# Kernel tuning notes

Hardware: AMD Instinct MI355X
Metric: run time of the kernel (lower is better)

The kernel has to match this reference:

```python
import jax, jax.numpy as jnp
import numpy as np

N_STATE = 64
N_LAYERS = 4
D_MODEL = 512
D_OUT = 256
BATCH = 16
SEQLEN = 2048


def setup_inputs() -> dict:
    key = jax.random.key(0)
    ks = jax.random.split(key, 16)
    H, N, nl = D_MODEL, N_STATE, N_LAYERS
    inp = {}
    inp["x"] = jax.random.normal(ks[0], (BATCH, SEQLEN, D_MODEL), dtype=jnp.float32)
    # encoder / decoder dense
    inp["enc_w"] = jax.random.normal(ks[1], (D_MODEL, D_MODEL), jnp.float32) / np.sqrt(D_MODEL)
    inp["enc_b"] = jnp.zeros((D_MODEL,), jnp.float32)
    inp["dec_w"] = jax.random.normal(ks[2], (D_MODEL, D_OUT), jnp.float32) / np.sqrt(D_MODEL)
    inp["dec_b"] = jnp.zeros((D_OUT,), jnp.float32)
    # per-layer LayerNorm
    inp["ln_scale"] = jnp.ones((nl, D_MODEL), jnp.float32)
    inp["ln_bias"] = jnp.zeros((nl, D_MODEL), jnp.float32)
    # per-layer S4 DPLR params (stored as real/imag float pairs)
    inp["lambda_re"] = -0.5 * jnp.ones((nl, H, N), jnp.float32)
    inp["lambda_im"] = jnp.broadcast_to(np.pi * jnp.arange(N, dtype=jnp.float32), (nl, H, N))
    inp["p_re"] = jax.random.normal(ks[3], (nl, H, N), jnp.float32) * 0.5
    inp["p_im"] = jax.random.normal(ks[4], (nl, H, N), jnp.float32) * 0.5
    inp["b_re"] = jax.random.normal(ks[5], (nl, H, N), jnp.float32) * 0.5
    inp["b_im"] = jax.random.normal(ks[6], (nl, H, N), jnp.float32) * 0.5
    inp["c_re"] = jax.random.normal(ks[7], (nl, H, N), jnp.float32) * 0.5
    inp["c_im"] = jax.random.normal(ks[8], (nl, H, N), jnp.float32) * 0.5
    inp["log_step"] = jax.random.uniform(ks[9], (nl, H), jnp.float32, minval=np.log(1e-3), maxval=np.log(1e-1))
    inp["d_param"] = jnp.ones((nl, H), jnp.float32)
    # per-layer output Dense
    inp["out_w"] = jax.random.normal(ks[10], (nl, D_MODEL, D_MODEL), jnp.float32) / np.sqrt(D_MODEL)
    inp["out_b"] = jnp.zeros((nl, D_MODEL), jnp.float32)
    return inp


def _layer_norm(x, scale, bias, eps=1e-6):
    mu = jnp.mean(x, axis=-1, keepdims=True)
    var = jnp.mean(jnp.square(x - mu), axis=-1, keepdims=True)
    return (x - mu) * jax.lax.rsqrt(var + eps) * scale + bias


def _kernel_dplr(Lam, P, B, C, step, L):
    # Lam,P,B,C: [H,N] complex64; step: [H] float32 -> K: [H,L] float32
    theta = (2.0 * np.pi / L) * jnp.arange(L, dtype=jnp.float32)
    Omega = jnp.exp(-1j * theta)                        # [L] roots of unity
    g = (2.0 / step)[:, None] * ((1.0 - Omega) / (1.0 + Omega))[None, :]  # [H,L]
    c = 2.0 / (1.0 + Omega)                             # [L]
    r = 1.0 / (g[:, :, None] - Lam[:, None, :])         # [H,L,N] resolvent (Cauchy)
    Cc, Pc = jnp.conj(C), jnp.conj(P)
    k00 = jnp.einsum("hn,hln->hl", Cc * B, r)
    k01 = jnp.einsum("hn,hln->hl", Cc * P, r)
    k10 = jnp.einsum("hn,hln->hl", Pc * B, r)
    k11 = jnp.einsum("hn,hln->hl", Pc * P, r)
    at_roots = c[None, :] * (k00 - k01 * (1.0 / (1.0 + k11)) * k10)  # [H,L]
    return jnp.fft.ifft(at_roots, n=L, axis=-1).real


def _s4_apply(u, Lam, P, B, C, step, D):
    # u: [Bt,L,H]; causal FFT convolution with kernel K[h,:] per channel
    L = u.shape[1]
    K = _kernel_dplr(Lam, P, B, C, step, L)             # [H,L]
    ud = jnp.fft.rfft(u, n=2 * L, axis=1)               # [Bt,L+1,H]
    Kd = jnp.fft.rfft(K, n=2 * L, axis=-1)              # [H,L+1]
    y = jnp.fft.irfft(ud * Kd.T[None], n=2 * L, axis=1)[:, :L]
    return y + D[None, None, :] * u


def reference(x, enc_w, enc_b, ln_scale, ln_bias, lambda_re, lambda_im,
              p_re, p_im, b_re, b_im, c_re, c_im, log_step, d_param,
              out_w, out_b, dec_w, dec_b):
    h = x @ enc_w + enc_b
    n_layers = ln_scale.shape[0]
    for i in range(n_layers):
        skip = h
        z = _layer_norm(h, ln_scale[i], ln_bias[i])
        Lam = lambda_re[i] + 1j * lambda_im[i]
        P = p_re[i] + 1j * p_im[i]
        B = b_re[i] + 1j * b_im[i]
        C = c_re[i] + 1j * c_im[i]
        z = _s4_apply(z, Lam, P, B, C, jnp.exp(log_step[i]), d_param[i])
        z = jax.nn.gelu(z)
        z = z @ out_w[i] + out_b[i]
        h = skip + z  # dropout=0.0 -> identity
    logits = h @ dec_w + dec_b
    return jax.nn.log_softmax(logits, axis=-1)
```

## Files before the change

kernel.cpp:

```cpp
#include <hip/hip_runtime.h>
#include <hip/hip_bf16.h>

#define NLAY 4
#define DH   512
#define NST  64
#define NB   16
#define SL   2048
#define NDO  256
#define BL   (NB*SL)
#define KDIM 512
#define TWOPI 6.283185307179586476925287

typedef unsigned short u16;
typedef __attribute__((ext_vector_type(8))) short  short8v;
typedef __attribute__((ext_vector_type(8))) unsigned short ushort8v;
typedef __attribute__((ext_vector_type(4))) float  f32x4;

#define RCPF(x) __builtin_amdgcn_rcpf(x)

__device__ __forceinline__ float bf2f(u16 v){
  union { unsigned u; float f; } x; x.u = ((unsigned)v) << 16; return x.f;
}
__device__ __forceinline__ u16 f2bf(float f){
  union { float f; unsigned u; } x; x.f = f;
  unsigned u = x.u;
  unsigned r = u + 0x7fffu + ((u >> 16) & 1u);
  return (u16)(r >> 16);
}
__device__ __forceinline__ void cmulw(float& xr, float& xi, float wr, float wi){
  float tr = xr*wr - xi*wi;
  xi = fmaf(xr, wi, xi*wr);
  xr = tr;
}
__device__ __forceinline__ float gelu_fast(float v){
  const float c0 = 0.7978845608028654f;
  float u = c0 * fmaf(0.044715f, v*v*v, v);
  return v * RCPF(1.0f + __expf(-2.0f * u));
}

template<int SGN>
__device__ __forceinline__ void dft4w(float& r0, float& i0, float& r1, float& i1,
                                      float& r2, float& i2, float& r3, float& i3){
  const float t0r = r0 + r2, t0i = i0 + i2;
  const float t1r = r0 - r2, t1i = i0 - i2;
  const float t2r = r1 + r3, t2i = i1 + i3;
  const float t3r = r1 - r3, t3i = i1 - i3;
  r0 = t0r + t2r; i0 = t0i + t2i;
  r2 = t0r - t2r; i2 = t0i - t2i;
  if (SGN < 0){ r1 = t1r + t3i; i1 = t1i - t3r; r3 = t1r - t3i; i3 = t1i + t3r; }
  else        { r1 = t1r - t3i; i1 = t1i + t3r; r3 = t1r + t3i; i3 = t1i - t3r; }
}

template<int SGN>
__device__ __forceinline__ void dft16(float* re, float* im){
#pragma unroll
  for (int b = 0; b < 4; b++)
    dft4w<SGN>(re[b], im[b], re[4+b], im[4+b], re[8+b], im[8+b], re[12+b], im[12+b]);
  const float C1 = 0.92387953251128675613f, S1_ = 0.38268343236508977172f;
  const float C2 = 0.70710678118654752440f;
  const float sg = (SGN < 0) ? -1.f : 1.f;
  cmulw(re[5],  im[5],   C1,  sg*S1_);
  cmulw(re[9],  im[9],   C2,  sg*C2);
  cmulw(re[13], im[13],  S1_, sg*C1);
  cmulw(re[6],  im[6],   C2,  sg*C2);
  cmulw(re[10], im[10],  0.f, sg*1.f);
  cmulw(re[14], im[14], -C2,  sg*C2);
  cmulw(re[7],  im[7],   S1_, sg*C1);
  cmulw(re[11], im[11], -C2,  sg*C2);
  cmulw(re[15], im[15], -C1,  sg*(-S1_));
#pragma unroll
  for (int c = 0; c < 4; c++)
    dft4w<SGN>(re[4*c], im[4*c], re[4*c+1], im[4*c+1], re[4*c+2], im[4*c+2], re[4*c+3], im[4*c+3]);
  float tr_, ti_;
#define SWP(A,B) tr_=re[A]; re[A]=re[B]; re[B]=tr_; ti_=im[A]; im[A]=im[B]; im[B]=ti_;
  SWP(1,4) SWP(2,8) SWP(3,12) SWP(6,9) SWP(7,13) SWP(11,14)
#undef SWP
}

__device__ __forceinline__ int cxpad(int i){ return i + (i >> 4) + ((i >> 8) << 1); }
#define CXSZ 4384

__device__ __forceinline__ void fwd4096(float* re, float* im, float2* cx, int t){
  dft16<-1>(re, im);
  const float a0 = -(float)(TWOPI/4096.0) * (float)t;
#pragma unroll
  for (int k = 0; k < 16; k++){
    if (k){ float sn = __sinf(a0*(float)k), cs = __cosf(a0*(float)k); cmulw(re[k], im[k], cs, sn); }
    cx[cxpad(t + 256*k)] = make_float2(re[k], im[k]);
  }
  __syncthreads();
  const int k1 = t >> 4, m2 = t & 15;
  const int b2 = k1*256 + m2;
#pragma unroll
  for (int j = 0; j < 16; j++){ float2 v = cx[cxpad(b2 + 16*j)]; re[j] = v.x; im[j] = v.y; }
  dft16<-1>(re, im);
  const float b0 = -(float)(TWOPI/256.0) * (float)m2;
#pragma unroll
  for (int k = 0; k < 16; k++){
    if (k){ float sn = __sinf(b0*(float)k), cs = __cosf(b0*(float)k); cmulw(re[k], im[k], cs, sn); }
    cx[cxpad(b2 + 16*k)] = make_float2(re[k], im[k]);
  }
  __syncthreads();
#pragma unroll
  for (int j = 0; j < 16; j++){ float2 v = cx[cxpad(16*t + j)]; re[j] = v.x; im[j] = v.y; }
  dft16<-1>(re, im);
}

__device__ __forceinline__ void inv4096(float* re, float* im, float2* cx, int t){
  dft16<1>(re, im);
#pragma unroll
  for (int j = 0; j < 16; j++) cx[cxpad(16*t + j)] = make_float2(re[j], im[j]);
  __syncthreads();
  const int k1 = t >> 4, m2 = t & 15;
  const int b2 = k1*256 + m2;
  const float b0 = (float)(TWOPI/256.0) * (float)m2;
#pragma unroll
  for (int k = 0; k < 16; k++){
    float2 v = cx[cxpad(b2 + 16*k)];
    re[k] = v.x; im[k] = v.y;
    if (k){ float sn = __sinf(b0*(float)k), cs = __cosf(b0*(float)k); cmulw(re[k], im[k], cs, sn); }
  }
  dft16<1>(re, im);
#pragma unroll
  for (int j = 0; j < 16; j++) cx[cxpad(b2 + 16*j)] = make_float2(re[j], im[j]);
  __syncthreads();
  const float a0 = (float)(TWOPI/4096.0) * (float)t;
#pragma unroll
  for (int k = 0; k < 16; k++){
    float2 v = cx[cxpad(t + 256*k)];
    re[k] = v.x; im[k] = v.y;
    if (k){ float sn = __sinf(a0*(float)k), cs = __cosf(a0*(float)k); cmulw(re[k], im[k], cs, sn); }
  }
  dft16<1>(re, im);
}

__global__ __launch_bounds__(256) void prep_k(
  const float* __restrict__ lam_re, const float* __restrict__ lam_im,
  const float* __restrict__ p_re,  const float* __restrict__ p_im,
  const float* __restrict__ b_re,  const float* __restrict__ b_im,
  const float* __restrict__ c_re,  const float* __restrict__ c_im,
  float4* __restrict__ cwA, float4* __restrict__ cwB, float* __restrict__ cwS)
{
  const int i = blockIdx.x * 256 + threadIdx.x;
  const float lr = lam_re[i], li = lam_im[i];
  const float pr = p_re[i],  pi = p_im[i];
  const float br = b_re[i],  bi = b_im[i];
  const float cr = c_re[i],  ci = c_im[i];
  cwA[i] = make_float4(lr, li, cr*br + ci*bi, cr*bi - ci*br);
  cwB[i] = make_float4(cr*pr + ci*pi, cr*pi - ci*pr, pr*br + pi*bi, pr*bi - pi*br);
  cwS[i] = pr*pr + pi*pi;
}

__global__ __launch_bounds__(256) void cauchy_k(
    const float4* __restrict__ cwA, const float4* __restrict__ cwB,
    const float* __restrict__ cwS, const float* __restrict__ lstep,
    float2* __restrict__ Kd)
{
  const int t = threadIdx.x;
  const int h = blockIdx.y, lay = blockIdx.z;
  const int l = blockIdx.x * 256 + t;
  const int wb = (lay*DH + h) * NST;
  const float stp = expf(lstep[lay*DH + h]);
  const float tw0 = 2.0f / stp;

  const float th = (float)(TWOPI/2048.0) * (float)l;
  const float sn = sinf(th), cs = cosf(th);
  const float omr = cs, omi = -sn;
  const float a1r = 1.f - omr, a1i = -omi;
  const float a2r = 1.f + omr, a2i =  omi;
  const float inv2 = RCPF(fmaf(a2r, a2r, a2i*a2i));
  const float gr = tw0 * fmaf(a1r, a2r,  a1i*a2i) * inv2;
  const float gi = tw0 * fmaf(a1i, a2r, -a1r*a2i) * inv2;
  const float clr = 2.f * a2r * inv2, cli = -2.f * a2i * inv2;

  float k00r=0.f,k00i=0.f,k01r=0.f,k01i=0.f,k10r=0.f,k10i=0.f,k11r=0.f,k11i=0.f;
#pragma unroll 4
  for (int n = 0; n < NST; n++){
    const float4 A  = cwA[wb + n];
    const float4 Bv = cwB[wb + n];
    const float w11 = cwS[wb + n];
    const float dr = gr - A.x, di = gi - A.y;
    const float s = RCPF(fmaf(dr, dr, di*di));
    const float ivr = dr * s, ivi = -di * s;
    k00r = fmaf(A.z, ivr, fmaf(-A.w, ivi, k00r)); k00i = fmaf(A.z, ivi, fmaf(A.w, ivr, k00i));
    k01r = fmaf(Bv.x,ivr, fmaf(-Bv.y,ivi, k01r)); k01i = fmaf(Bv.x,ivi, fmaf(Bv.y,ivr, k01i));
    k10r = fmaf(Bv.z,ivr, fmaf(-Bv.w,ivi, k10r)); k10i = fmaf(Bv.z,ivi, fmaf(Bv.w,ivr, k10i));
    k11r = fmaf(w11, ivr, k11r);                  k11i = fmaf(w11, ivi, k11i);
  }
  const float d1r = 1.f + k11r, d1i = k11i;
  const float idn = RCPF(fmaf(d1r, d1r, d1i*d1i));
  const float wr = k01r*k10r - k01i*k10i, wi = k01r*k10i + k01i*k10r;
  const float vr = fmaf(wr, d1r,  wi*d1i) * idn;
  const float vi = fmaf(wi, d1r, -wr*d1i) * idn;
  const float sr = k00r - vr, si = k00i - vi;
  Kd[(size_t)(lay*DH + h) * 4096 + l] =
      make_float2(clr*sr - cli*si, fmaf(clr, si, cli*sr));
}

__global__ __launch_bounds__(256) void kdfft_k(float2* __restrict__ Kd){
  __shared__ float  ar[SL], ai[SL];
  __shared__ float2 cx[CXSZ];
  const int t = threadIdx.x;
  const size_t base = (size_t)blockIdx.x * 4096;
#pragma unroll
  for (int q = 0; q < 8; q++){
    const int l = t + 256*q;
    float2 v = Kd[base + l];
    const int brv = __brev((unsigned)l) >> 21;
    ar[brv] = v.x; ai[brv] = v.y;
  }
  __syncthreads();

  for (int s = 0; s < 11; s++){
    const int half = 1 << s;
    const float fac = (float)(TWOPI) / (float)(2 << s);
#pragma unroll
    for (int q = 0; q < 4; q++){
      const int v = t + 256*q;
      const int pos = v & (half - 1);
      const int i0 = ((v >> s) << (s+1)) + pos;
      const int i1 = i0 + half;
      const float ang = fac * (float)pos;
      const float wc = __cosf(ang), ws = __sinf(ang);
      const float xr = ar[i1], xi = ai[i1];
      const float tr = wc*xr - ws*xi, ti = fmaf(wc, xi, ws*xr);
      const float ur_ = ar[i0], ui_ = ai[i0];
      ar[i0] = ur_ + tr; ai[i0] = ui_ + ti;
      ar[i1] = ur_ - tr; ai[i1] = ui_ - ti;
    }
    __syncthreads();
  }

  float re[16], im[16];
#pragma unroll
  for (int j = 0; j < 16; j++){
    re[j] = (j < 8) ? ar[t + 256*j] * (1.0f/2048.f) : 0.f;
    im[j] = 0.f;
  }
  fwd4096(re, im, cx, t);
  float2* kp = Kd + base + 16*t;
#pragma unroll
  for (int k = 0; k < 16; k += 2)
    *(float4*)(kp + k) = make_float4(re[k], im[k], re[k+1], im[k+1]);
}

__global__ __launch_bounds__(256) void wconv_k(const float* __restrict__ src,
    u16* __restrict__ dst, int K, int N){
  __shared__ u16 tile[64][72];
  const size_t mb = (size_t)blockIdx.z * K * N;
  const int k0 = blockIdx.x * 64, n0 = blockIdx.y * 64;
  const int r = threadIdx.x >> 2, c4 = (threadIdx.x & 3) * 16;
  const float* s = src + mb + (size_t)(k0 + r) * N + n0 + c4;
  float4 f0 = *(const float4*)s, f1 = *(const float4*)(s+4);
  float4 f2 = *(const float4*)(s+8), f3 = *(const float4*)(s+12);
  tile[c4+0][r]=f2bf(f0.x); tile[c4+1][r]=f2bf(f0.y); tile[c4+2][r]=f2bf(f0.z); tile[c4+3][r]=f2bf(f0.w);
  tile[c4+4][r]=f2bf(f1.x); tile[c4+5][r]=f2bf(f1.y); tile[c4+6][r]=f2bf(f1.z); tile[c4+7][r]=f2bf(f1.w);
  tile[c4+8][r]=f2bf(f2.x); tile[c4+9][r]=f2bf(f2.y); tile[c4+10][r]=f2bf(f2.z); tile[c4+11][r]=f2bf(f2.w);
  tile[c4+12][r]=f2bf(f3.x); tile[c4+13][r]=f2bf(f3.y); tile[c4+14][r]=f2bf(f3.z); tile[c4+15][r]=f2bf(f3.w);
  __syncthreads();
  u16* d = dst + mb + (size_t)(n0 + r) * K + k0 + c4;
  *(ushort8v*)d       = *(const ushort8v*)&tile[r][c4];
  *(ushort8v*)(d + 8) = *(const ushort8v*)&tile[r][c4 + 8];
}

__global__ __launch_bounds__(256) void ln_k(const float* __restrict__ hsrc,
    const float* __restrict__ gam, const float* __restrict__ bet,
    u16* __restrict__ zdst){
  const int row = blockIdx.x * 4 + (threadIdx.x >> 6);
  const int lane = threadIdx.x & 63;
  const float* p = hsrc + (size_t)row * DH + lane * 8;
  float4 a = *(const float4*)p, b = *(const float4*)(p + 4);
  float s  = (a.x + a.y) + (a.z + a.w) + (b.x + b.y) + (b.z + b.w);
  float sq = a.x*a.x + a.y*a.y + a.z*a.z + a.w*a.w
           + b.x*b.x + b.y*b.y + b.z*b.z + b.w*b.w;
#pragma unroll
  for (int o = 32; o; o >>= 1){ s += __shfl_xor(s, o); sq += __shfl_xor(sq, o); }
  const float mu = s * (1.0f/DH);
  const float rs = rsqrtf(sq * (1.0f/DH) - mu*mu + 1e-6f);
  const float4 g0 = *(const float4*)(gam + lane*8), g1 = *(const float4*)(gam + lane*8 + 4);
  const float4 t0 = *(const float4*)(bet + lane*8), t1 = *(const float4*)(bet + lane*8 + 4);
  ushort8v o;
  o[0] = f2bf(fmaf((a.x - mu)*rs, g0.x, t0.x));
  o[1] = f2bf(fmaf((a.y - mu)*rs, g0.y, t0.y));
  o[2] = f2bf(fmaf((a.z - mu)*rs, g0.z, t0.z));
  o[3] = f2bf(fmaf((a.w - mu)*rs, g0.w, t0.w));
  o[4] = f2bf(fmaf((b.x - mu)*rs, g1.x, t1.x));
  o[5] = f2bf(fmaf((b.y - mu)*rs, g1.y, t1.y));
  o[6] = f2bf(fmaf((b.z - mu)*rs, g1.z, t1.z));
  o[7] = f2bf(fmaf((b.w - mu)*rs, g1.w, t1.w));
  *(ushort8v*)(zdst + (size_t)row * DH + lane*8) = o;
}

__global__ __launch_bounds__(256) void transp_k(const u16* __restrict__ z,
                                                u16* __restrict__ zT){
  __shared__ u16 tile[64][72];
  const int bz = blockIdx.z;
  const int l0 = blockIdx.x * 64, h0 = blockIdx.y * 64;
  const int r = threadIdx.x >> 2, c4 = (threadIdx.x & 3) * 16;
  const u16* src = z + ((size_t)bz * SL + l0 + r) * DH + h0 + c4;
  ushort8v v0 = *(const ushort8v*)src;
  ushort8v v1 = *(const ushort8v*)(src + 8);
#pragma unroll
  for (int j = 0; j < 8; j++){ tile[c4 + j][r] = v0[j]; tile[c4 + 8 + j][r] = v1[j]; }
  __syncthreads();
  u16* dst = zT + ((size_t)bz * DH + h0 + r) * SL + l0 + c4;
  *(ushort8v*)dst       = *(const ushort8v*)&tile[r][c4];
  *(ushort8v*)(dst + 8) = *(const ushort8v*)&tile[r][c4 + 8];
}

__global__ __launch_bounds__(256) void s4conv_k(
    const u16* __restrict__ zT, const float2* __restrict__ Kd,
    const float* __restrict__ dpar, u16* __restrict__ yT)
{
  __shared__ float2 cx[CXSZ];
  const int t = threadIdx.x;
  const int wg = blockIdx.x;
  const int h = wg & 511, bp = wg >> 9;
  const u16* r1 = zT + ((size_t)(2*bp) * DH + h) * SL;
  const u16* r2 = r1 + (size_t)DH * SL;
  float ur1[8], ur2[8];
  float re[16], im[16];
#pragma unroll
  for (int j = 0; j < 8; j++){
    ur1[j] = bf2f(r1[t + 256*j]);
    ur2[j] = bf2f(r2[t + 256*j]);
    re[j] = ur1[j]; im[j] = ur2[j];
  }
#pragma unroll
  for (int j = 8; j < 16; j++){ re[j] = 0.f; im[j] = 0.f; }

  fwd4096(re, im, cx, t);

  const float2* kp = Kd + (size_t)h * 4096 + 16*t;
#pragma unroll
  for (int k = 0; k < 16; k += 2){
    float4 w2 = *(const float4*)(kp + k);
    cmulw(re[k],   im[k],   w2.x, w2.y);
    cmulw(re[k+1], im[k+1], w2.z, w2.w);
  }

  inv4096(re, im, cx, t);

  const float Dv = dpar[h];
  u16* y1 = yT + ((size_t)(2*bp) * DH + h) * SL;
  u16* y2 = y1 + (size_t)DH * SL;
#pragma unroll
  for (int j = 0; j < 8; j++){
    float v1 = fmaf(re[j], (1.0f/4096.f), Dv * ur1[j]);
    float v2 = fmaf(im[j], (1.0f/4096.f), Dv * ur2[j]);
    y1[t + 256*j] = f2bf(gelu_fast(v1));
    y2[t + 256*j] = f2bf(gelu_fast(v2));
  }
}

template<int AMODE, bool RESID>
__global__ __launch_bounds__(256) void gemm_k(
    const void* __restrict__ Aptr, const u16* __restrict__ Wt,
    const float* __restrict__ bias,
    const float* __restrict__ resid, float* __restrict__ Cout,
    int Mb, int N)
{
  __shared__ u16 As[128][40];
  __shared__ u16 Bs[128][40];
  const int t = threadIdx.x;
  const int n0 = blockIdx.x * 128, m0 = blockIdx.y * 128, bb = blockIdx.z;
  const int lane = t & 63, wv = t >> 6;
  const int wm = (wv >> 1) * 64, wn = (wv & 1) * 64;
  f32x4 acc[4][4];
#pragma unroll
  for (int mi = 0; mi < 4; mi++)
#pragma unroll
    for (int ni = 0; ni < 4; ni++) acc[mi][ni] = {0.f, 0.f, 0.f, 0.f};

  const u16*  Ab = (const u16*)Aptr;
  const float* Af = (const float*)Aptr;
  const size_t Abase = (AMODE == 1) ? (size_t)bb * KDIM * Mb : 0;

  for (int k0 = 0; k0 < KDIM; k0 += 32){
    __syncthreads();
    if (AMODE == 1){
      const int kk = t >> 3, ch = t & 7;
      const u16* srca = Ab + Abase + (size_t)(k0 + kk) * Mb + m0 + ch*16;
      ushort8v v0 = *(const ushort8v*)srca;
      ushort8v v1 = *(const ushort8v*)(srca + 8);
      const int col = (kk & 7) | (((kk >> 3) ^ (ch & 3)) << 3);
#pragma unroll
      for (int i = 0; i < 8; i++){
        As[ch*16 + i][col]     = (u16)v0[i];
        As[ch*16 + 8 + i][col] = (u16)v1[i];
      }
    } else if (AMODE == 0){
      const int r = t >> 1, kh = (t & 1) << 4;
      const u16* srca = Ab + (size_t)(m0 + r) * KDIM + k0 + kh;
      ushort8v v0 = *(const ushort8v*)srca;
      ushort8v v1 = *(const ushort8v*)(srca + 8);
      const int s3 = (r >> 4) & 3;
      const int c0 = (((kh >> 3) ^ s3) << 3);
      const int c1 = ((((kh >> 3) + 1) ^ s3) << 3);
      *(ushort8v*)&As[r][c0] = v0;
      *(ushort8v*)&As[r][c1] = v1;
    } else {
      const int r = t >> 1, kh = (t & 1) << 4;
      const float* sf = Af + (size_t)(m0 + r) * KDIM + k0 + kh;
      float4 f0 = *(const float4*)sf,     f1 = *(const float4*)(sf + 4);
      float4 f2 = *(const float4*)(sf+8), f3 = *(const float4*)(sf + 12);
      ushort8v v0, v1;
      v0[0]=f2bf(f0.x); v0[1]=f2bf(f0.y); v0[2]=f2bf(f0.z); v0[3]=f2bf(f0.w);
      v0[4]=f2bf(f1.x); v0[5]=f2bf(f1.y); v0[6]=f2bf(f1.z); v0[7]=f2bf(f1.w);
      v1[0]=f2bf(f2.x); v1[1]=f2bf(f2.y); v1[2]=f2bf(f2.z); v1[3]=f2bf(f2.w);
      v1[4]=f2bf(f3.x); v1[5]=f2bf(f3.y); v1[6]=f2bf(f3.z); v1[7]=f2bf(f3.w);
      const int s3 = (r >> 4) & 3;
      const int c0 = (((kh >> 3) ^ s3) << 3);
      const int c1 = ((((kh >> 3) + 1) ^ s3) << 3);
      *(ushort8v*)&As[r][c0] = v0;
      *(ushort8v*)&As[r][c1] = v1;
    }
    {
      const int r = t >> 1, kh = (t & 1) << 4;
      const u16* srcb = Wt + (size_t)(n0 + r) * KDIM + k0 + kh;
      ushort8v v0 = *(const ushort8v*)srcb;
      ushort8v v1 = *(const ushort8v*)(srcb + 8);
      const int s3 = (r >> 4) & 3;
      const int c0 = (((kh >> 3) ^ s3) << 3);
      const int c1 = ((((kh >> 3) + 1) ^ s3) << 3);
      *(ushort8v*)&Bs[r][c0] = v0;
      *(ushort8v*)&Bs[r][c1] = v1;
    }
    __syncthreads();

    const int ko = (lane >> 4) * 8;
    const int fr = lane & 15;
    short8v af[4], bf[4];
#pragma unroll
    for (int mi = 0; mi < 4; mi++){
      const int col = (((ko >> 3) ^ (((wm >> 4) + mi) & 3)) << 3);
      af[mi] = *(const short8v*)&As[wm + mi*16 + fr][col];
    }
#pragma unroll
    for (int ni = 0; ni < 4; ni++){
      const int col = (((ko >> 3) ^ (((wn >> 4) + ni) & 3)) << 3);
      bf[ni] = *(const short8v*)&Bs[wn + ni*16 + fr][col];
    }
#pragma unroll
    for (int mi = 0; mi < 4; mi++)
#pragma unroll
      for (int ni = 0; ni < 4; ni++)
        acc[mi][ni] = __builtin_amdgcn_mfma_f32_16x16x32_bf16(af[mi], bf[ni], acc[mi][ni], 0, 0, 0);
  }

  const int fr = lane & 15;
  const int rq = (lane >> 4) * 4;
#pragma unroll
  for (int mi = 0; mi < 4; mi++){
#pragma unroll
    for (int ni = 0; ni < 4; ni++){
      const int gn = n0 + wn + ni*16 + fr;
      const float bs = bias[gn];
#pragma unroll
      for (int q = 0; q < 4; q++){
        const int gm = m0 + wm + mi*16 + rq + q;
        const size_t idx = ((size_t)bb * Mb + gm) * N + gn;
        float v = acc[mi][ni][q] + bs;
        if (RESID) v += resid[idx];
        Cout[idx] = v;
      }
    }
  }
}

__global__ __launch_bounds__(256) void lsm_k(float* __restrict__ o){
  const int row = blockIdx.x * 4 + (threadIdx.x >> 6);
  const int lane = threadIdx.x & 63;
  float* p = o + (size_t)row * NDO + lane * 4;
  float4 v = *(const float4*)p;
  float mx = fmaxf(fmaxf(v.x, v.y), fmaxf(v.z, v.w));
#pragma unroll
  for (int q = 32; q; q >>= 1) mx = fmaxf(mx, __shfl_xor(mx, q));
  float e = __expf(v.x - mx) + __expf(v.y - mx) + __expf(v.z - mx) + __expf(v.w - mx);
#pragma unroll
  for (int q = 32; q; q >>= 1) e += __shfl_xor(e, q);
  const float lse = mx + __logf(e);
  v.x -= lse; v.y -= lse; v.z -= lse; v.w -= lse;
  *(float4*)p = v;
}

extern "C" void kernel_launch(void* const* d_in, const int* in_sizes, int n_in,
                              void* d_out, int out_size, void* d_ws, size_t ws_size,
                              hipStream_t stream)
{
  (void)in_sizes; (void)n_in; (void)out_size; (void)ws_size;
  const float* x      = (const float*)d_in[0];
  const float* enc_w  = (const float*)d_in[1];
  const float* enc_b  = (const float*)d_in[2];
  const float* dec_w  = (const float*)d_in[3];
  const float* dec_b  = (const float*)d_in[4];
  const float* ln_s   = (const float*)d_in[5];
  const float* ln_b   = (const float*)d_in[6];
  const float* lam_re = (const float*)d_in[7];
  const float* lam_im = (const float*)d_in[8];
  const float* p_re   = (const float*)d_in[9];
  const float* p_im   = (const float*)d_in[10];
  const float* b_re   = (const float*)d_in[11];
  const float* b_im   = (const float*)d_in[12];
  const float* c_re   = (const float*)d_in[13];
  const float* c_im   = (const float*)d_in[14];
  const float* lstep  = (const float*)d_in[15];
  const float* d_par  = (const float*)d_in[16];
  const float* out_w  = (const float*)d_in[17];
  const float* out_b  = (const float*)d_in[18];

  char* ws = (char*)d_ws;
  float*  hbuf = (float*)(ws);
  u16*    abf  = (u16*)  (ws + (size_t)67108864);
  u16*    zT   = (u16*)  (ws + (size_t)67108864 + 33554432);
  u16*    yT   = (u16*)  (ws + (size_t)67108864 + 2*33554432);
  float2* Kd   = (float2*)(ws + (size_t)67108864 + 3*33554432);
  u16*    Wt   = (u16*)  (ws + (size_t)67108864 + 3*33554432 + 67108864);
  u16*    WtEnc = Wt;
  u16*    WtOut = Wt + 262144;
  u16*    WtDec = Wt + 262144*5;
  float*  outp = (float*)d_out;

  float4* cwA = (float4*)d_out;
  float4* cwB = cwA + 131072;
  float*  cwS = (float*)(cwB + 131072);

  prep_k<<<dim3(NLAY*DH*NST/256), 256, 0, stream>>>(lam_re, lam_im, p_re, p_im,
                                                    b_re, b_im, c_re, c_im, cwA, cwB, cwS);
  wconv_k<<<dim3(8, 8, 1), 256, 0, stream>>>(enc_w, WtEnc, KDIM, DH);
  wconv_k<<<dim3(8, 8, NLAY), 256, 0, stream>>>(out_w, WtOut, KDIM, DH);
  wconv_k<<<dim3(8, 4, 1), 256, 0, stream>>>(dec_w, WtDec, KDIM, NDO);
  cauchy_k<<<dim3(8, DH, NLAY), 256, 0, stream>>>(cwA, cwB, cwS, lstep, Kd);
  kdfft_k<<<dim3(NLAY*DH), 256, 0, stream>>>(Kd);
  gemm_k<2,false><<<dim3(DH/128, BL/128, 1), 256, 0, stream>>>(
      x, WtEnc, enc_b, nullptr, hbuf, BL, DH);
  for (int i = 0; i < NLAY; i++){
    ln_k<<<dim3(BL/4), 256, 0, stream>>>(hbuf, ln_s + i*DH, ln_b + i*DH, abf);
    transp_k<<<dim3(SL/64, DH/64, NB), 256, 0, stream>>>(abf, zT);
    s4conv_k<<<dim3((NB/2)*DH), 256, 0, stream>>>(
        zT, Kd + (size_t)i*DH*4096, d_par + i*DH, yT);
    gemm_k<1,true><<<dim3(DH/128, SL/128, NB), 256, 0, stream>>>(
        yT, WtOut + (size_t)i*262144, out_b + i*DH, hbuf, hbuf, SL, DH);
  }
  gemm_k<2,false><<<dim3(NDO/128, BL/128, 1), 256, 0, stream>>>(
      hbuf, WtDec, dec_b, nullptr, outp, BL, NDO);
  lsm_k<<<dim3(BL/4), 256, 0, stream>>>(outp);
}
```

Baseline: 848.7 us.

## Fuse LayerNorm with transpose and simplify Cauchy kernel via tangent form

LayerNorm and the transpose into channel-major layout become one kernel that stages a 32-row tile in swizzled shared memory, so the bf16 intermediate buffer is no longer written and read back. The Cauchy kernel evaluation now uses the fact that the bilinear-transform frequency is purely imaginary (tan form), which drops the real-part subtraction and simplifies the output factor. Each thread also computes four frequencies, so every weight load is reused four times. The LayerNorm output is now quantized to bf16 before normalization, which changes rounding slightly, and the larger per-thread register state may lower occupancy.

```diff
diff --git a/kernel.cpp b/kernel.cpp
--- a/kernel.cpp
+++ b/kernel.cpp
@@ -158,43 +158,59 @@
 {
   const int t = threadIdx.x;
   const int h = blockIdx.y, lay = blockIdx.z;
-  const int l = blockIdx.x * 256 + t;
+  const int lb = blockIdx.x * 256 + t;
   const int wb = (lay*DH + h) * NST;
-  const float stp = expf(lstep[lay*DH + h]);
-  const float tw0 = 2.0f / stp;
-
-  const float th = (float)(TWOPI/2048.0) * (float)l;
-  const float sn = sinf(th), cs = cosf(th);
-  const float omr = cs, omi = -sn;
-  const float a1r = 1.f - omr, a1i = -omi;
-  const float a2r = 1.f + omr, a2i =  omi;
-  const float inv2 = RCPF(fmaf(a2r, a2r, a2i*a2i));
-  const float gr = tw0 * fmaf(a1r, a2r,  a1i*a2i) * inv2;
-  const float gi = tw0 * fmaf(a1i, a2r, -a1r*a2i) * inv2;
-  const float clr = 2.f * a2r * inv2, cli = -2.f * a2i * inv2;
-
-  float k00r=0.f,k00i=0.f,k01r=0.f,k01i=0.f,k10r=0.f,k10i=0.f,k11r=0.f,k11i=0.f;
-#pragma unroll 4
+  const float tw0 = 2.0f * expf(-lstep[lay*DH + h]);
+
+  float T[4], gi[4];
+#pragma unroll
+  for (int j = 0; j < 4; j++){
+    float sn, cs;
+    sincosf((float)(TWOPI/4096.0) * (float)(lb + 512*j), &sn, &cs);
+    T[j] = sn * RCPF(cs);
+    gi[j] = tw0 * T[j];
+  }
+
+  float k00r[4]={0,0,0,0}, k00i[4]={0,0,0,0};
+  float k01r[4]={0,0,0,0}, k01i[4]={0,0,0,0};
+  float k10r[4]={0,0,0,0}, k10i[4]={0,0,0,0};
+  float k11r[4]={0,0,0,0}, k11i[4]={0,0,0,0};
+
+#pragma unroll 2
   for (int n = 0; n < NST; n++){
     const float4 A  = cwA[wb + n];
     const float4 Bv = cwB[wb + n];
     const float w11 = cwS[wb + n];
-    const float dr = gr - A.x, di = gi - A.y;
-    const float s = RCPF(fmaf(dr, dr, di*di));
-    const float ivr = dr * s, ivi = -di * s;
-    k00r = fmaf(A.z, ivr, fmaf(-A.w, ivi, k00r)); k00i = fmaf(A.z, ivi, fmaf(A.w, ivr, k00i));
-    k01r = fmaf(Bv.x,ivr, fmaf(-Bv.y,ivi, k01r)); k01i = fmaf(Bv.x,ivi, fmaf(Bv.y,ivr, k01i));
-    k10r = fmaf(Bv.z,ivr, fmaf(-Bv.w,ivi, k10r)); k10i = fmaf(Bv.z,ivi, fmaf(Bv.w,ivr, k10i));
-    k11r = fmaf(w11, ivr, k11r);                  k11i = fmaf(w11, ivi, k11i);
-  }
-  const float d1r = 1.f + k11r, d1i = k11i;
-  const float idn = RCPF(fmaf(d1r, d1r, d1i*d1i));
-  const float wr = k01r*k10r - k01i*k10i, wi = k01r*k10i + k01i*k10r;
-  const float vr = fmaf(wr, d1r,  wi*d1i) * idn;
-  const float vi = fmaf(wi, d1r, -wr*d1i) * idn;
-  const float sr = k00r - vr, si = k00i - vi;
-  Kd[(size_t)(lay*DH + h) * 4096 + l] =
-      make_float2(clr*sr - cli*si, fmaf(clr, si, cli*sr));
+    const float nlr = -A.x;
+    const float dr2 = A.x * A.x;
+#pragma unroll
+    for (int j = 0; j < 4; j++){
+      const float di = gi[j] - A.y;
+      const float sI = RCPF(fmaf(di, di, dr2));
+      const float ivr = nlr * sI, ivi = -di * sI;
+      k00r[j] = fmaf(A.z,  ivr, fmaf(-A.w,  ivi, k00r[j]));
+      k00i[j] = fmaf(A.z,  ivi, fmaf( A.w,  ivr, k00i[j]));
+      k01r[j] = fmaf(Bv.x, ivr, fmaf(-Bv.y, ivi, k01r[j]));
+      k01i[j] = fmaf(Bv.x, ivi, fmaf( Bv.y, ivr, k01i[j]));
+      k10r[j] = fmaf(Bv.z, ivr, fmaf(-Bv.w, ivi, k10r[j]));
+      k10i[j] = fmaf(Bv.z, ivi, fmaf( Bv.w, ivr, k10i[j]));
+      k11r[j] = fmaf(w11,  ivr, k11r[j]);
+      k11i[j] = fmaf(w11,  ivi, k11i[j]);
+    }
+  }
+
+  float2* kp = Kd + (size_t)(lay*DH + h) * 4096;
+#pragma unroll
+  for (int j = 0; j < 4; j++){
+    const float d1r = 1.f + k11r[j], d1i = k11i[j];
+    const float idn = RCPF(fmaf(d1r, d1r, d1i*d1i));
+    const float wr = k01r[j]*k10r[j] - k01i[j]*k10i[j];
+    const float wi = k01r[j]*k10i[j] + k01i[j]*k10r[j];
+    const float vr = fmaf(wr, d1r,  wi*d1i) * idn;
+    const float vi = fmaf(wi, d1r, -wr*d1i) * idn;
+    const float sr = k00r[j] - vr, si = k00i[j] - vi;
+    kp[lb + 512*j] = make_float2(fmaf(-T[j], si, sr), fmaf(T[j], sr, si));
+  }
 }
 
 __global__ __launch_bounds__(256) void kdfft_k(float2* __restrict__ Kd){
@@ -263,49 +279,66 @@
   *(ushort8v*)(d + 8) = *(const ushort8v*)&tile[r][c4 + 8];
 }
 
-__global__ __launch_bounds__(256) void ln_k(const float* __restrict__ hsrc,
+#define LTILE 32
+__device__ __forceinline__ int lnswz(int h){ return ((h >> 1) + (h >> 6)) & 3; }
+
+__global__ __launch_bounds__(256) void lnt_k(const float* __restrict__ hsrc,
     const float* __restrict__ gam, const float* __restrict__ bet,
-    u16* __restrict__ zdst){
-  const int row = blockIdx.x * 4 + (threadIdx.x >> 6);
-  const int lane = threadIdx.x & 63;
-  const float* p = hsrc + (size_t)row * DH + lane * 8;
-  float4 a = *(const float4*)p, b = *(const float4*)(p + 4);
-  float s  = (a.x + a.y) + (a.z + a.w) + (b.x + b.y) + (b.z + b.w);
-  float sq = a.x*a.x + a.y*a.y + a.z*a.z + a.w*a.w
-           + b.x*b.x + b.y*b.y + b.z*b.z + b.w*b.w;
-#pragma unroll
-  for (int o = 32; o; o >>= 1){ s += __shfl_xor(s, o); sq += __shfl_xor(sq, o); }
-  const float mu = s * (1.0f/DH);
-  const float rs = rsqrtf(sq * (1.0f/DH) - mu*mu + 1e-6f);
-  const float4 g0 = *(const float4*)(gam + lane*8), g1 = *(const float4*)(gam + lane*8 + 4);
-  const float4 t0 = *(const float4*)(bet + lane*8), t1 = *(const float4*)(bet + lane*8 + 4);
-  ushort8v o;
-  o[0] = f2bf(fmaf((a.x - mu)*rs, g0.x, t0.x));
-  o[1] = f2bf(fmaf((a.y - mu)*rs, g0.y, t0.y));
-  o[2] = f2bf(fmaf((a.z - mu)*rs, g0.z, t0.z));
-  o[3] = f2bf(fmaf((a.w - mu)*rs, g0.w, t0.w));
-  o[4] = f2bf(fmaf((b.x - mu)*rs, g1.x, t1.x));
-  o[5] = f2bf(fmaf((b.y - mu)*rs, g1.y, t1.y));
-  o[6] = f2bf(fmaf((b.z - mu)*rs, g1.z, t1.z));
-  o[7] = f2bf(fmaf((b.w - mu)*rs, g1.w, t1.w));
-  *(ushort8v*)(zdst + (size_t)row * DH + lane*8) = o;
-}
-
-__global__ __launch_bounds__(256) void transp_k(const u16* __restrict__ z,
-                                                u16* __restrict__ zT){
-  __shared__ u16 tile[64][72];
-  const int bz = blockIdx.z;
-  const int l0 = blockIdx.x * 64, h0 = blockIdx.y * 64;
-  const int r = threadIdx.x >> 2, c4 = (threadIdx.x & 3) * 16;
-  const u16* src = z + ((size_t)bz * SL + l0 + r) * DH + h0 + c4;
-  ushort8v v0 = *(const ushort8v*)src;
-  ushort8v v1 = *(const ushort8v*)(src + 8);
-#pragma unroll
-  for (int j = 0; j < 8; j++){ tile[c4 + j][r] = v0[j]; tile[c4 + 8 + j][r] = v1[j]; }
-  __syncthreads();
-  u16* dst = zT + ((size_t)bz * DH + h0 + r) * SL + l0 + c4;
-  *(ushort8v*)dst       = *(const ushort8v*)&tile[r][c4];
-  *(ushort8v*)(dst + 8) = *(const ushort8v*)&tile[r][c4 + 8];
+    u16* __restrict__ zT){
+  __shared__ u16 tile[DH][LTILE];
+  __shared__ float smu[LTILE], srs[LTILE];
+  const int t = threadIdx.x;
+  const int b = blockIdx.y, l0 = blockIdx.x * LTILE;
+  const int r = t >> 3, hb = (t & 7) * 64;
+  const float* p = hsrc + ((size_t)b * SL + l0 + r) * DH + hb;
+  float s = 0.f, sq = 0.f;
+#pragma unroll
+  for (int j4 = 0; j4 < 16; j4++){
+    float4 v = *(const float4*)(p + j4*4);
+    s  += (v.x + v.y) + (v.z + v.w);
+    sq += v.x*v.x + v.y*v.y + v.z*v.z + v.w*v.w;
+    const int h0 = hb + j4*4;
+    tile[h0+0][r ^ (lnswz(h0+0) << 3)] = f2bf(v.x);
+    tile[h0+1][r ^ (lnswz(h0+1) << 3)] = f2bf(v.y);
+    tile[h0+2][r ^ (lnswz(h0+2) << 3)] = f2bf(v.z);
+    tile[h0+3][r ^ (lnswz(h0+3) << 3)] = f2bf(v.w);
+  }
+  s  += __shfl_xor(s, 1);  sq += __shfl_xor(sq, 1);
+  s  += __shfl_xor(s, 2);  sq += __shfl_xor(sq, 2);
+  s  += __shfl_xor(s, 4);  sq += __shfl_xor(sq, 4);
+  if ((t & 7) == 0){
+    const float mu = s * (1.0f/DH);
+    smu[r] = mu;
+    srs[r] = rsqrtf(sq * (1.0f/DH) - mu*mu + 1e-6f);
+  }
+  __syncthreads();
+
+#pragma unroll
+  for (int hh = 0; hh < 2; hh++){
+    const int h = t + hh*256;
+    const float g = gam[h], be = bet[h];
+    const int sw = lnswz(h);
+    u16* dst = zT + ((size_t)b * DH + h) * SL + l0;
+#pragma unroll
+    for (int og = 0; og < 4; og++){
+      const int lg = og ^ sw;
+      ushort8v v = *(const ushort8v*)&tile[h][og*8];
+      const float4 m0 = *(const float4*)&smu[lg*8];
+      const float4 m1 = *(const float4*)&smu[lg*8 + 4];
+      const float4 r0 = *(const float4*)&srs[lg*8];
+      const float4 r1 = *(const float4*)&srs[lg*8 + 4];
+      ushort8v o;
+      o[0] = f2bf(fmaf(bf2f((u16)v[0]) - m0.x, r0.x*g, be));
+      o[1] = f2bf(fmaf(bf2f((u16)v[1]) - m0.y, r0.y*g, be));
+      o[2] = f2bf(fmaf(bf2f((u16)v[2]) - m0.z, r0.z*g, be));
+      o[3] = f2bf(fmaf(bf2f((u16)v[3]) - m0.w, r0.w*g, be));
+      o[4] = f2bf(fmaf(bf2f((u16)v[4]) - m1.x, r1.x*g, be));
+      o[5] = f2bf(fmaf(bf2f((u16)v[5]) - m1.y, r1.y*g, be));
+      o[6] = f2bf(fmaf(bf2f((u16)v[6]) - m1.z, r1.z*g, be));
+      o[7] = f2bf(fmaf(bf2f((u16)v[7]) - m1.w, r1.w*g, be));
+      *(ushort8v*)(dst + lg*8) = o;
+    }
+  }
 }
 
 __global__ __launch_bounds__(256) void s4conv_k(
@@ -511,7 +544,6 @@
 
   char* ws = (char*)d_ws;
   float*  hbuf = (float*)(ws);
-  u16*    abf  = (u16*)  (ws + (size_t)67108864);
   u16*    zT   = (u16*)  (ws + (size_t)67108864 + 33554432);
   u16*    yT   = (u16*)  (ws + (size_t)67108864 + 2*33554432);
   float2* Kd   = (float2*)(ws + (size_t)67108864 + 3*33554432);
@@ -530,13 +562,12 @@
   wconv_k<<<dim3(8, 8, 1), 256, 0, stream>>>(enc_w, WtEnc, KDIM, DH);
   wconv_k<<<dim3(8, 8, NLAY), 256, 0, stream>>>(out_w, WtOut, KDIM, DH);
   wconv_k<<<dim3(8, 4, 1), 256, 0, stream>>>(dec_w, WtDec, KDIM, NDO);
-  cauchy_k<<<dim3(8, DH, NLAY), 256, 0, stream>>>(cwA, cwB, cwS, lstep, Kd);
+  cauchy_k<<<dim3(2, DH, NLAY), 256, 0, stream>>>(cwA, cwB, cwS, lstep, Kd);
   kdfft_k<<<dim3(NLAY*DH), 256, 0, stream>>>(Kd);
   gemm_k<2,false><<<dim3(DH/128, BL/128, 1), 256, 0, stream>>>(
       x, WtEnc, enc_b, nullptr, hbuf, BL, DH);
   for (int i = 0; i < NLAY; i++){
-    ln_k<<<dim3(BL/4), 256, 0, stream>>>(hbuf, ln_s + i*DH, ln_b + i*DH, abf);
-    transp_k<<<dim3(SL/64, DH/64, NB), 256, 0, stream>>>(abf, zT);
+    lnt_k<<<dim3(SL/LTILE, NB), 256, 0, stream>>>(hbuf, ln_s + i*DH, ln_b + i*DH, zT);
     s4conv_k<<<dim3((NB/2)*DH), 256, 0, stream>>>(
         zT, Kd + (size_t)i*DH*4096, d_par + i*DH, yT);
     gemm_k<1,true><<<dim3(DH/128, SL/128, NB), 256, 0, stream>>>(
```

Measured after the change: 838.2 us. No clear change (-1.2%).
